# Optimization experiments

Measured on AMD Instinct MI355X. Metric: run time of the kernel, lower is better.

## Reference

```python
import jax, jax.numpy as jnp
import numpy as np

D_MODEL = 1024
N_HEADS = 16
D_HEAD = 64
TOTAL = N_HEADS * D_HEAD


def setup_inputs() -> dict:
    key = jax.random.key(0)
    k1, k2, k3 = jax.random.split(key, 3)
    x = jax.random.normal(k1, (2, 2048, D_MODEL), dtype=jnp.float32)
    W_qkv = jax.random.normal(k2, (3 * TOTAL, D_MODEL), dtype=jnp.float32) * 0.02
    W_out = jax.random.normal(k3, (D_MODEL, TOTAL), dtype=jnp.float32) * 0.02
    return {"x": x, "W_qkv": W_qkv, "W_out": W_out}


def reference(x, W_qkv, W_out):
    B, T, D = x.shape
    scale = D_HEAD ** -0.5
    qkv = jnp.einsum('btd,ed->bte', x, W_qkv)  # [B,T,3*TOTAL]
    q, k, v = jnp.split(qkv, 3, axis=-1)
    def heads(t):
        return t.reshape(B, T, N_HEADS, D_HEAD).transpose(0, 2, 1, 3)  # [B,H,T,Dh]
    q, k, v = heads(q), heads(k), heads(v)
    scores = jnp.einsum('bhqd,bhkd->bhqk', q, k) * scale
    causal = jnp.tril(jnp.ones((T, T), dtype=bool))
    scores = jnp.where(causal[None, None], scores, -jnp.inf)
    attn = jax.nn.softmax(scores, axis=-1)
    out = jnp.einsum('bhqk,bhkd->bhqd', attn, v)
    out = out.transpose(0, 2, 1, 3).reshape(B, T, TOTAL)
    return jnp.einsum('bte,de->btd', out, W_out)
```

## Files before the change

### kernel.cpp

```cpp
#include <hip/hip_runtime.h>
#include <hip/hip_bf16.h>

typedef __attribute__((ext_vector_type(4))) float f32x4;
typedef __attribute__((ext_vector_type(8))) short s16x8;
typedef __attribute__((ext_vector_type(4))) short s16x4;

#define DEV static __device__ __forceinline__

DEV unsigned short f2bf(float f) {
    unsigned int u = __builtin_bit_cast(unsigned int, f);
    u += 0x7fffu + ((u >> 16) & 1u);
    return (unsigned short)(u >> 16);
}

#if __has_builtin(__builtin_amdgcn_exp2f)
#define EXP2(x) __builtin_amdgcn_exp2f(x)
#else
#define EXP2(x) exp2f(x)
#endif

DEV unsigned int pack2(float a, float b) {
#if __has_builtin(__builtin_amdgcn_perm)
    return __builtin_amdgcn_perm(__builtin_bit_cast(unsigned int, b),
                                 __builtin_bit_cast(unsigned int, a), 0x07060302u);
#else
    return (__builtin_bit_cast(unsigned int, a) >> 16) |
           (__builtin_bit_cast(unsigned int, b) & 0xffff0000u);
#endif
}

DEV s16x8 ld8(const unsigned short* p) {
    s16x4 lo = *(const s16x4*)(p);
    s16x4 hi = *(const s16x4*)(p + 4);
    return __builtin_shufflevector(lo, hi, 0, 1, 2, 3, 4, 5, 6, 7);
}
DEV s16x8 ld8a(const unsigned short* p) { return *(const s16x8*)p; }

DEV f32x4 mfma16(s16x8 a, s16x8 b, f32x4 c) {
    return __builtin_amdgcn_mfma_f32_16x16x32_bf16(a, b, c, 0, 0, 0);
}

DEV void glds16(const unsigned short* g, unsigned short* l) {
    __builtin_amdgcn_global_load_lds(
        (const __attribute__((address_space(1))) unsigned int*)g,
        (__attribute__((address_space(3))) unsigned int*)l, 16, 0, 0);
}

__global__ __launch_bounds__(256) void convf2b2(
        const float* __restrict__ s0, unsigned short* __restrict__ d0, int n40,
        const float* __restrict__ s1, unsigned short* __restrict__ d1, int n41) {
    int i = blockIdx.x * 256 + threadIdx.x;
    if (i < n40) {
        float4 v = ((const float4*)s0)[i];
        s16x4 o = {(short)f2bf(v.x), (short)f2bf(v.y), (short)f2bf(v.z), (short)f2bf(v.w)};
        ((s16x4*)d0)[i] = o;
    } else if (i - n40 < n41) {
        int j = i - n40;
        float4 v = ((const float4*)s1)[j];
        s16x4 o = {(short)f2bf(v.x), (short)f2bf(v.y), (short)f2bf(v.z), (short)f2bf(v.w)};
        ((s16x4*)d1)[j] = o;
    }
}

__global__ __launch_bounds__(256) void convf2b(const float* __restrict__ s,
                                               unsigned short* __restrict__ d, int n4) {
    int i = blockIdx.x * 256 + threadIdx.x;
    if (i < n4) {
        float4 v = ((const float4*)s)[i];
        s16x4 o = {(short)f2bf(v.x), (short)f2bf(v.y), (short)f2bf(v.z), (short)f2bf(v.w)};
        ((s16x4*)d)[i] = o;
    }
}

__global__ __launch_bounds__(512) void qkv_gemm(
        const unsigned short* __restrict__ Xb, const unsigned short* __restrict__ Wq,
        unsigned short* __restrict__ q_ws, unsigned short* __restrict__ k_ws,
        unsigned short* __restrict__ v_ws) {
    __shared__ unsigned short As[2][128 * 32];
    __shared__ unsigned short Bs[2][128 * 32];
    const int tid = threadIdx.x, lane = tid & 63, wave = tid >> 6;
    const int l15 = lane & 15, l4 = lane >> 4;
    const int wm = (wave >> 1) * 32, wn = (wave & 1) * 64;
    const int m0 = blockIdx.y * 128, n0 = blockIdx.x * 128;

    f32x4 acc[2][4];
    for (int i = 0; i < 2; i++)
        for (int j = 0; j < 4; j++) acc[i][j] = (f32x4){0.f, 0.f, 0.f, 0.f};

    const unsigned short* aptr = &Xb[(size_t)(m0 + wave * 16 + (lane >> 2)) * 1024 + (lane & 3) * 8];
    const unsigned short* bptr = &Wq[(size_t)(n0 + wave * 16 + (lane >> 2)) * 1024 + (lane & 3) * 8];

    for (int k0 = 0; k0 < 1024; k0 += 64) {
        __syncthreads();
        for (int c = 0; c < 2; c++) {
            glds16(aptr + k0 + c * 32, &As[c][(wave * 16) * 32]);
            glds16(bptr + k0 + c * 32, &Bs[c][(wave * 16) * 32]);
        }
        __syncthreads();
        for (int c = 0; c < 2; c++) {
            s16x8 af[2], bf[4];
            for (int mt = 0; mt < 2; mt++) af[mt] = ld8a(&As[c][(wm + mt * 16 + l15) * 32 + l4 * 8]);
            for (int nt = 0; nt < 4; nt++) bf[nt] = ld8a(&Bs[c][(wn + nt * 16 + l15) * 32 + l4 * 8]);
            for (int mt = 0; mt < 2; mt++)
                for (int nt = 0; nt < 4; nt++)
                    acc[mt][nt] = mfma16(af[mt], bf[nt], acc[mt][nt]);
        }
    }

    const int gnb = n0 + wn;
    const int which = gnb >> 10, h = (gnb >> 6) & 15;
    const int bidx = m0 >> 11, tb = m0 & 2047;
    if (which == 2) {
        unsigned short* dst = v_ws + (size_t)(bidx * 16 + h) * 64 * 2048;
        for (int mt = 0; mt < 2; mt++) {
            int t = tb + wm + mt * 16 + l4 * 4;
            for (int nt = 0; nt < 4; nt++) {
                int dh = nt * 16 + l15;
                s16x4 pp;
                for (int r = 0; r < 4; r++) pp[r] = (short)f2bf(acc[mt][nt][r]);
                *(s16x4*)&dst[(size_t)dh * 2048 + t] = pp;
            }
        }
    } else {
        unsigned short* dst = ((which == 0) ? q_ws : k_ws) + (size_t)(bidx * 16 + h) * 2048 * 64;
        const float sc = (which == 0) ? 0.18033688f : 1.0f;
        for (int mt = 0; mt < 2; mt++) {
            int t0 = tb + wm + mt * 16 + l4 * 4;
            for (int nt = 0; nt < 4; nt++) {
                int dh = nt * 16 + l15;
                for (int r = 0; r < 4; r++)
                    dst[(size_t)(t0 + r) * 64 + dh] = f2bf(acc[mt][nt][r] * sc);
            }
        }
    }
}

__global__ __launch_bounds__(512, 4) void attn(
        const unsigned short* __restrict__ q_ws, const unsigned short* __restrict__ k_ws,
        const unsigned short* __restrict__ v_ws, unsigned short* __restrict__ ao) {
    constexpr int LDP = 68;
    __shared__ unsigned short Ks[3][2][64 * 32];
    __shared__ unsigned short Vt[3][2][64 * 32];
    __shared__ unsigned short Ps[8 * 16 * LDP];
    const int tid = threadIdx.x, lane = tid & 63, wave = tid >> 6;
    const int l15 = lane & 15, l4 = lane >> 4;
    const int xf = (l15 >> 1) & 3;

    const int id = blockIdx.x;
    const int bh8 = id & 7, rest = id >> 3;
    const int qq = rest & 15, g = rest >> 4;
    const int bh = bh8 + 8 * g, b = bh >> 4, h = bh & 15;
    const int p = (g < 2) ? qq : 15 - qq;
    const int qrow = ((wave < 4) ? (31 - p) : p) * 64 + (wave & 3) * 16;
    const int nt = 32 - p;

    const size_t base = (size_t)bh * 2048 * 64;
    const unsigned short* vtb = v_ws + (size_t)bh * 64 * 2048;
    unsigned short* Pw = &Ps[wave * 16 * LDP];

    const int seg = wave >> 1, hf = wave & 1;
    const int srow = lane >> 2;
    const int scol = ((lane & 3) ^ ((lane >> 3) & 3)) * 8;
    const unsigned short* kg = &k_ws[base + (size_t)(seg * 16 + srow) * 64 + hf * 32 + scol];
    const unsigned short* vg = &vtb[(size_t)(seg * 16 + srow) * 2048 + hf * 32 + scol];
    unsigned short* kld = &Ks[0][hf][(seg * 16) * 32];
    unsigned short* vld = &Vt[0][hf][(seg * 16) * 32];
    const unsigned short* krd = &Ks[0][0][0];
    const unsigned short* vrd = &Vt[0][0][0];

    s16x8 qf[2];
    for (int c = 0; c < 2; c++)
        qf[c] = ld8a(&q_ws[base + (size_t)(qrow + l15) * 64 + c * 32 + l4 * 8]);
    asm volatile("s_waitcnt vmcnt(0)" ::: "memory");

    f32x4 o[4];
    for (int i = 0; i < 4; i++) o[i] = (f32x4){0.f, 0.f, 0.f, 0.f};
    float lsum = 0.f;

    glds16(kg, kld);
    glds16(vg, vld);
    glds16(kg + 4096, kld + 4096);
    glds16(vg + 64, vld + 4096);

    int cur = 0;
    for (int r = 0; r < nt; ++r) {
        if (r + 1 < nt) asm volatile("s_waitcnt vmcnt(2)" ::: "memory");
        else            asm volatile("s_waitcnt vmcnt(0)" ::: "memory");
        __builtin_amdgcn_s_barrier();
        if (r + 2 < nt) {
            const int nb = (cur == 0) ? 2 : cur - 1;
            glds16(kg + (size_t)(r + 2) * 4096, kld + nb * 4096);
            glds16(vg + (r + 2) * 64,           vld + nb * 4096);
        }
        const int k0 = r * 64;
        if (k0 < qrow + 16) {
            const unsigned short* kb = krd + cur * 4096;
            const unsigned short* vb = vrd + cur * 4096;
            f32x4 st[4];
            for (int ks = 0; ks < 4; ks++) st[ks] = (f32x4){0.f, 0.f, 0.f, 0.f};
            __builtin_amdgcn_s_setprio(1);
            for (int c = 0; c < 2; c++)
                for (int ks = 0; ks < 4; ks++) {
                    s16x8 kf = ld8a(&kb[c * 2048 + (ks * 16 + l15) * 32 + (l4 ^ xf) * 8]);
                    st[ks] = mfma16(kf, qf[c], st[ks]);
                }
            __builtin_amdgcn_s_setprio(0);

            if (k0 + 63 > qrow) {
                int qg = qrow + l15;
                for (int ks = 0; ks < 4; ks++)
                    for (int rr = 0; rr < 4; rr++) {
                        int kgi = k0 + ks * 16 + l4 * 4 + rr;
                        if (kgi > qg) st[ks][rr] = -1e30f;
                    }
            }
            float part = 0.f;
            for (int ks = 0; ks < 4; ks++) {
                float p0 = EXP2(st[ks][0]);
                float p1 = EXP2(st[ks][1]);
                float p2 = EXP2(st[ks][2]);
                float p3 = EXP2(st[ks][3]);
                part += (p0 + p1) + (p2 + p3);
                unsigned int u0 = pack2(p0, p1), u1 = pack2(p2, p3);
                *(uint2*)&Pw[l15 * LDP + ks * 16 + l4 * 4] = (uint2){u0, u1};
            }
            lsum += part;

            s16x8 pf[2];
            for (int c = 0; c < 2; c++)
                pf[c] = ld8(&Pw[l15 * LDP + c * 32 + l4 * 8]);
            __builtin_amdgcn_s_setprio(1);
            for (int c = 0; c < 2; c++)
                for (int ds = 0; ds < 4; ds++) {
                    s16x8 vf = ld8a(&vb[c * 2048 + (ds * 16 + l15) * 32 + (l4 ^ xf) * 8]);
                    o[ds] = mfma16(vf, pf[c], o[ds]);
                }
            __builtin_amdgcn_s_setprio(0);
        }
        cur = (cur == 2) ? 0 : cur + 1;
    }

    float t = lsum;
    t += __shfl_xor(t, 16, 64);
    t += __shfl_xor(t, 32, 64);
    float inv = 1.f / t;
    for (int ds = 0; ds < 4; ds++) {
        s16x4 pp;
        for (int r = 0; r < 4; r++) pp[r] = (short)f2bf(o[ds][r] * inv);
        *(s16x4*)&Pw[l15 * LDP + ds * 16 + l4 * 4] = pp;
    }
    int qr = lane >> 2, qt = lane & 3;
    size_t orow = ((size_t)b * 2048 + qrow + qr) * 1024 + h * 64 + qt * 16;
    *(s16x8*)&ao[orow]     = ld8(&Pw[qr * LDP + qt * 16]);
    *(s16x8*)&ao[orow + 8] = ld8(&Pw[qr * LDP + qt * 16 + 8]);
}

__global__ __launch_bounds__(256) void out_gemm(
        const unsigned short* __restrict__ A, const unsigned short* __restrict__ Bm,
        float* __restrict__ OUT) {
    __shared__ unsigned short As[2][128 * 32];
    __shared__ unsigned short Bs[2][64 * 32];
    const int tid = threadIdx.x, lane = tid & 63, wave = tid >> 6;
    const int l15 = lane & 15, l4 = lane >> 4;
    const int wm = wave * 32;
    const int m0 = blockIdx.y * 128, n0 = blockIdx.x * 64;

    f32x4 acc[2][4];
    for (int i = 0; i < 2; i++)
        for (int j = 0; j < 4; j++) acc[i][j] = (f32x4){0.f, 0.f, 0.f, 0.f};

    const unsigned short* aptr = &A[(size_t)(m0 + wave * 32 + (lane >> 2)) * 1024 + (lane & 3) * 8];
    const unsigned short* bptr = &Bm[(size_t)(n0 + wave * 16 + (lane >> 2)) * 1024 + (lane & 3) * 8];

    for (int k0 = 0; k0 < 1024; k0 += 64) {
        __syncthreads();
        for (int c = 0; c < 2; c++) {
            glds16(aptr + k0 + c * 32, &As[c][(wave * 32) * 32]);
            glds16(aptr + k0 + c * 32 + 16 * 1024, &As[c][(wave * 32 + 16) * 32]);
            glds16(bptr + k0 + c * 32, &Bs[c][(wave * 16) * 32]);
        }
        __syncthreads();
        for (int c = 0; c < 2; c++) {
            s16x8 af[2], bf[4];
            for (int mt = 0; mt < 2; mt++) af[mt] = ld8a(&As[c][(wm + mt * 16 + l15) * 32 + l4 * 8]);
            for (int nt = 0; nt < 4; nt++) bf[nt] = ld8a(&Bs[c][(nt * 16 + l15) * 32 + l4 * 8]);
            for (int mt = 0; mt < 2; mt++)
                for (int nt = 0; nt < 4; nt++)
                    acc[mt][nt] = mfma16(af[mt], bf[nt], acc[mt][nt]);
        }
    }

    for (int mt = 0; mt < 2; mt++)
        for (int nt = 0; nt < 4; nt++)
            for (int r = 0; r < 4; r++) {
                int gm = m0 + wm + mt * 16 + l4 * 4 + r;
                int gn = n0 + nt * 16 + l15;
                OUT[(size_t)gm * 1024 + gn] = acc[mt][nt][r];
            }
}

extern "C" void kernel_launch(void* const* d_in, const int* in_sizes, int n_in,
                              void* d_out, int out_size, void* d_ws, size_t ws_size,
                              hipStream_t stream) {
    (void)in_sizes; (void)n_in; (void)out_size; (void)ws_size;
    const float* x    = (const float*)d_in[0];
    const float* Wqkv = (const float*)d_in[1];
    const float* Wout = (const float*)d_in[2];
    float* out = (float*)d_out;

    unsigned short* q_ws = (unsigned short*)d_ws;
    unsigned short* k_ws = q_ws + (size_t)4 * 1024 * 1024;
    unsigned short* v_ws = k_ws + (size_t)4 * 1024 * 1024;
    unsigned short* xb   = v_ws + (size_t)4 * 1024 * 1024;
    unsigned short* ao   = xb;
    unsigned short* wqb  = (unsigned short*)d_out;
    unsigned short* wob  = q_ws;

    const int n4x = 2 * 2048 * 1024 / 4, n4w = 3072 * 1024 / 4;
    convf2b2<<<(n4x + n4w + 255) / 256, 256, 0, stream>>>(x, xb, n4x, Wqkv, wqb, n4w);
    qkv_gemm<<<dim3(24, 32), 512, 0, stream>>>(xb, wqb, q_ws, k_ws, v_ws);
    attn<<<dim3(512), 512, 0, stream>>>(q_ws, k_ws, v_ws, ao);
    convf2b<<<1024, 256, 0, stream>>>(Wout, wob, 1024 * 1024 / 4);
    out_gemm<<<dim3(16, 32), 256, 0, stream>>>(ao, wob, out);
}
```

Before: 165.0 us.

## Enlarge QKV GEMM tiles to 256x256 with swizzled LDS and pipelined loads

Rewrites the QKV projection GEMM to use 256x256 output tiles with a K-step of 64 and double-buffered LDS. Global-to-LDS loads for the next step are issued while MFMAs run on the current one, using explicit vmcnt waits, barriers and setprio. An XOR swizzle on the LDS layout avoids bank conflicts, and the 1D grid of 192 blocks is remapped to group tiles for L2 reuse. The goal is higher arithmetic intensity and better overlap of memory and compute. The cost is 128 KB of LDS per block, more accumulator registers, and only 192 blocks, which may leave some CUs idle.

```diff
diff --git a/kernel.cpp b/kernel.cpp
--- a/kernel.cpp
+++ b/kernel.cpp
@@ -72,64 +72,152 @@
     }
 }
 
-__global__ __launch_bounds__(512) void qkv_gemm(
+__global__ __launch_bounds__(512, 2) void qkv_gemm(
         const unsigned short* __restrict__ Xb, const unsigned short* __restrict__ Wq,
         unsigned short* __restrict__ q_ws, unsigned short* __restrict__ k_ws,
         unsigned short* __restrict__ v_ws) {
-    __shared__ unsigned short As[2][128 * 32];
-    __shared__ unsigned short Bs[2][128 * 32];
+    __shared__ unsigned short As[2][256 * 64];
+    __shared__ unsigned short Bs[2][256 * 64];
     const int tid = threadIdx.x, lane = tid & 63, wave = tid >> 6;
     const int l15 = lane & 15, l4 = lane >> 4;
-    const int wm = (wave >> 1) * 32, wn = (wave & 1) * 64;
-    const int m0 = blockIdx.y * 128, n0 = blockIdx.x * 128;
-
-    f32x4 acc[2][4];
-    for (int i = 0; i < 2; i++)
+    const int wr = wave >> 2, wc = wave & 3;
+    const int swz = (blockIdx.x & 7) * 24 + (blockIdx.x >> 3);
+    const int m0 = (swz / 12) * 256, n0 = (swz % 12) * 256;
+
+    f32x4 acc[8][4];
+#pragma unroll
+    for (int i = 0; i < 8; i++)
+#pragma unroll
         for (int j = 0; j < 4; j++) acc[i][j] = (f32x4){0.f, 0.f, 0.f, 0.f};
 
-    const unsigned short* aptr = &Xb[(size_t)(m0 + wave * 16 + (lane >> 2)) * 1024 + (lane & 3) * 8];
-    const unsigned short* bptr = &Wq[(size_t)(n0 + wave * 16 + (lane >> 2)) * 1024 + (lane & 3) * 8];
-
-    for (int k0 = 0; k0 < 1024; k0 += 64) {
-        __syncthreads();
-        for (int c = 0; c < 2; c++) {
-            glds16(aptr + k0 + c * 32, &As[c][(wave * 16) * 32]);
-            glds16(bptr + k0 + c * 32, &Bs[c][(wave * 16) * 32]);
-        }
-        __syncthreads();
-        for (int c = 0; c < 2; c++) {
-            s16x8 af[2], bf[4];
-            for (int mt = 0; mt < 2; mt++) af[mt] = ld8a(&As[c][(wm + mt * 16 + l15) * 32 + l4 * 8]);
-            for (int nt = 0; nt < 4; nt++) bf[nt] = ld8a(&Bs[c][(wn + nt * 16 + l15) * 32 + l4 * 8]);
-            for (int mt = 0; mt < 2; mt++)
-                for (int nt = 0; nt < 4; nt++)
-                    acc[mt][nt] = mfma16(af[mt], bf[nt], acc[mt][nt]);
-        }
-    }
-
-    const int gnb = n0 + wn;
+    const int srow = lane >> 3, sslot = (lane & 7) ^ srow;
+    const unsigned short* aG = &Xb[(size_t)(m0 + wave * 32 + srow) * 1024 + sslot * 8];
+    const unsigned short* bG = &Wq[(size_t)(n0 + wave * 32 + srow) * 1024 + sslot * 8];
+
+#pragma unroll
+    for (int g = 0; g < 4; g++) glds16(aG + g * 8 * 1024, &As[0][(wave * 32 + g * 8) * 64]);
+#pragma unroll
+    for (int g = 0; g < 4; g++) glds16(bG + g * 8 * 1024, &Bs[0][(wave * 32 + g * 8) * 64]);
+
+    const int xro = l15 & 7;
+    s16x8 bf[4];
+    for (int t = 0; t < 16; ++t) {
+        const unsigned short* Ab = &As[t & 1][0];
+        const unsigned short* Bb = &Bs[t & 1][0];
+        unsigned short* Al = &As[(t & 1) ^ 1][0];
+        unsigned short* Bl = &Bs[(t & 1) ^ 1][0];
+
+        if (t < 15) {
+            const unsigned short* ag = aG + (size_t)(t + 1) * 64;
+#pragma unroll
+            for (int g = 0; g < 4; g++)
+                glds16(ag + g * 8 * 1024, &Al[(wave * 32 + g * 8) * 64]);
+            asm volatile("s_waitcnt vmcnt(4)" ::: "memory");
+        } else {
+            asm volatile("s_waitcnt vmcnt(0)" ::: "memory");
+        }
+        __builtin_amdgcn_s_barrier();
+        {
+            s16x8 af[4];
+#pragma unroll
+            for (int ii = 0; ii < 4; ii++)
+                af[ii] = ld8a(&Ab[(wr * 128 + ii * 16 + l15) * 64 + ((l4 ^ xro) * 8)]);
+#pragma unroll
+            for (int j = 0; j < 4; j++)
+                bf[j] = ld8a(&Bb[(wc * 64 + j * 16 + l15) * 64 + ((l4 ^ xro) * 8)]);
+            __builtin_amdgcn_s_setprio(1);
+#pragma unroll
+            for (int ii = 0; ii < 4; ii++)
+#pragma unroll
+                for (int j = 0; j < 4; j++) acc[ii][j] = mfma16(af[ii], bf[j], acc[ii][j]);
+            __builtin_amdgcn_s_setprio(0);
+        }
+        __builtin_amdgcn_s_barrier();
+
+        {
+            if (t < 15) {
+                const unsigned short* bg = bG + (size_t)(t + 1) * 64;
+#pragma unroll
+                for (int g = 0; g < 4; g++)
+                    glds16(bg + g * 8 * 1024, &Bl[(wave * 32 + g * 8) * 64]);
+            }
+            s16x8 af[4];
+#pragma unroll
+            for (int ii = 0; ii < 4; ii++)
+                af[ii] = ld8a(&Ab[(wr * 128 + (4 + ii) * 16 + l15) * 64 + ((l4 ^ xro) * 8)]);
+            __builtin_amdgcn_s_barrier();
+            __builtin_amdgcn_s_setprio(1);
+#pragma unroll
+            for (int ii = 0; ii < 4; ii++)
+#pragma unroll
+                for (int j = 0; j < 4; j++) acc[4 + ii][j] = mfma16(af[ii], bf[j], acc[4 + ii][j]);
+            __builtin_amdgcn_s_setprio(0);
+        }
+        __builtin_amdgcn_s_barrier();
+
+        {
+            s16x8 af[4];
+#pragma unroll
+            for (int ii = 0; ii < 4; ii++)
+                af[ii] = ld8a(&Ab[(wr * 128 + ii * 16 + l15) * 64 + (((4 + l4) ^ xro) * 8)]);
+#pragma unroll
+            for (int j = 0; j < 4; j++)
+                bf[j] = ld8a(&Bb[(wc * 64 + j * 16 + l15) * 64 + (((4 + l4) ^ xro) * 8)]);
+            __builtin_amdgcn_s_barrier();
+            __builtin_amdgcn_s_setprio(1);
+#pragma unroll
+            for (int ii = 0; ii < 4; ii++)
+#pragma unroll
+                for (int j = 0; j < 4; j++) acc[ii][j] = mfma16(af[ii], bf[j], acc[ii][j]);
+            __builtin_amdgcn_s_setprio(0);
+        }
+        __builtin_amdgcn_s_barrier();
+
+        {
+            s16x8 af[4];
+#pragma unroll
+            for (int ii = 0; ii < 4; ii++)
+                af[ii] = ld8a(&Ab[(wr * 128 + (4 + ii) * 16 + l15) * 64 + (((4 + l4) ^ xro) * 8)]);
+            __builtin_amdgcn_s_barrier();
+            __builtin_amdgcn_s_setprio(1);
+#pragma unroll
+            for (int ii = 0; ii < 4; ii++)
+#pragma unroll
+                for (int j = 0; j < 4; j++) acc[4 + ii][j] = mfma16(af[ii], bf[j], acc[4 + ii][j]);
+            __builtin_amdgcn_s_setprio(0);
+        }
+        __builtin_amdgcn_s_barrier();
+    }
+
+    const int gnb = n0 + wc * 64;
     const int which = gnb >> 10, h = (gnb >> 6) & 15;
     const int bidx = m0 >> 11, tb = m0 & 2047;
     if (which == 2) {
         unsigned short* dst = v_ws + (size_t)(bidx * 16 + h) * 64 * 2048;
-        for (int mt = 0; mt < 2; mt++) {
-            int t = tb + wm + mt * 16 + l4 * 4;
-            for (int nt = 0; nt < 4; nt++) {
-                int dh = nt * 16 + l15;
+#pragma unroll
+        for (int i = 0; i < 8; i++) {
+            int tq = tb + wr * 128 + i * 16 + l4 * 4;
+#pragma unroll
+            for (int j = 0; j < 4; j++) {
+                int dh = j * 16 + l15;
                 s16x4 pp;
-                for (int r = 0; r < 4; r++) pp[r] = (short)f2bf(acc[mt][nt][r]);
-                *(s16x4*)&dst[(size_t)dh * 2048 + t] = pp;
+#pragma unroll
+                for (int r = 0; r < 4; r++) pp[r] = (short)f2bf(acc[i][j][r]);
+                *(s16x4*)&dst[(size_t)dh * 2048 + tq] = pp;
             }
         }
     } else {
         unsigned short* dst = ((which == 0) ? q_ws : k_ws) + (size_t)(bidx * 16 + h) * 2048 * 64;
         const float sc = (which == 0) ? 0.18033688f : 1.0f;
-        for (int mt = 0; mt < 2; mt++) {
-            int t0 = tb + wm + mt * 16 + l4 * 4;
-            for (int nt = 0; nt < 4; nt++) {
-                int dh = nt * 16 + l15;
+#pragma unroll
+        for (int i = 0; i < 8; i++) {
+            int t0 = tb + wr * 128 + i * 16 + l4 * 4;
+#pragma unroll
+            for (int j = 0; j < 4; j++) {
+                int dh = j * 16 + l15;
+#pragma unroll
                 for (int r = 0; r < 4; r++)
-                    dst[(size_t)(t0 + r) * 64 + dh] = f2bf(acc[mt][nt][r] * sc);
+                    dst[(size_t)(t0 + r) * 64 + dh] = f2bf(acc[i][j][r] * sc);
             }
         }
     }
@@ -318,7 +406,7 @@
 
     const int n4x = 2 * 2048 * 1024 / 4, n4w = 3072 * 1024 / 4;
     convf2b2<<<(n4x + n4w + 255) / 256, 256, 0, stream>>>(x, xb, n4x, Wqkv, wqb, n4w);
-    qkv_gemm<<<dim3(24, 32), 512, 0, stream>>>(xb, wqb, q_ws, k_ws, v_ws);
+    qkv_gemm<<<dim3(192), 512, 0, stream>>>(xb, wqb, q_ws, k_ws, v_ws);
     attn<<<dim3(512), 512, 0, stream>>>(q_ws, k_ws, v_ws, ao);
     convf2b<<<1024, 256, 0, stream>>>(Wout, wob, 1024 * 1024 / 4);
     out_gemm<<<dim3(16, 32), 256, 0, stream>>>(ao, wob, out);
```

Result: slower. 184.3 us (+11.7%).

## Process 32 query rows per wave in attention and fold Wout conversion into prologue

Applied to the files above, without the earlier changes.

The attention kernel now gives each wave two 16-row query subtiles, so 128 query rows per block, and halves the grid to 256 blocks. Each K and V fragment read from LDS now feeds two MFMAs, which reuses shared-memory loads and halves global K/V staging per query row. The price is roughly double the accumulator and score registers, lower occupancy (launch bounds drop to 2 blocks) and a bigger P buffer. Separately, when the workspace is large enough, the W_out fp32-to-bf16 conversion is merged into the first conversion kernel to remove one launch.

```diff
diff --git a/kernel.cpp b/kernel.cpp
--- a/kernel.cpp
+++ b/kernel.cpp
@@ -46,9 +46,10 @@
         (__attribute__((address_space(3))) unsigned int*)l, 16, 0, 0);
 }
 
-__global__ __launch_bounds__(256) void convf2b2(
+__global__ __launch_bounds__(256) void convf2b3(
         const float* __restrict__ s0, unsigned short* __restrict__ d0, int n40,
-        const float* __restrict__ s1, unsigned short* __restrict__ d1, int n41) {
+        const float* __restrict__ s1, unsigned short* __restrict__ d1, int n41,
+        const float* __restrict__ s2, unsigned short* __restrict__ d2, int n42) {
     int i = blockIdx.x * 256 + threadIdx.x;
     if (i < n40) {
         float4 v = ((const float4*)s0)[i];
@@ -59,6 +60,11 @@
         float4 v = ((const float4*)s1)[j];
         s16x4 o = {(short)f2bf(v.x), (short)f2bf(v.y), (short)f2bf(v.z), (short)f2bf(v.w)};
         ((s16x4*)d1)[j] = o;
+    } else if (i - n40 - n41 < n42) {
+        int j = i - n40 - n41;
+        float4 v = ((const float4*)s2)[j];
+        s16x4 o = {(short)f2bf(v.x), (short)f2bf(v.y), (short)f2bf(v.z), (short)f2bf(v.w)};
+        ((s16x4*)d2)[j] = o;
     }
 }
 
@@ -135,28 +141,28 @@
     }
 }
 
-__global__ __launch_bounds__(512, 4) void attn(
+__global__ __launch_bounds__(512, 2) void attn(
         const unsigned short* __restrict__ q_ws, const unsigned short* __restrict__ k_ws,
         const unsigned short* __restrict__ v_ws, unsigned short* __restrict__ ao) {
     constexpr int LDP = 68;
     __shared__ unsigned short Ks[3][2][64 * 32];
     __shared__ unsigned short Vt[3][2][64 * 32];
-    __shared__ unsigned short Ps[8 * 16 * LDP];
+    __shared__ unsigned short Ps[8 * 32 * LDP];
     const int tid = threadIdx.x, lane = tid & 63, wave = tid >> 6;
     const int l15 = lane & 15, l4 = lane >> 4;
     const int xf = (l15 >> 1) & 3;
 
     const int id = blockIdx.x;
     const int bh8 = id & 7, rest = id >> 3;
-    const int qq = rest & 15, g = rest >> 4;
+    const int p = rest & 7, g = rest >> 3;
     const int bh = bh8 + 8 * g, b = bh >> 4, h = bh & 15;
-    const int p = (g < 2) ? qq : 15 - qq;
-    const int qrow = ((wave < 4) ? (31 - p) : p) * 64 + (wave & 3) * 16;
-    const int nt = 32 - p;
+    const int chunk = (wave < 4) ? (15 - p) : p;
+    const int qrow = chunk * 128 + (wave & 3) * 32;
+    const int nt = 2 * (16 - p);
 
     const size_t base = (size_t)bh * 2048 * 64;
     const unsigned short* vtb = v_ws + (size_t)bh * 64 * 2048;
-    unsigned short* Pw = &Ps[wave * 16 * LDP];
+    unsigned short* Pw = &Ps[wave * 32 * LDP];
 
     const int seg = wave >> 1, hf = wave & 1;
     const int srow = lane >> 2;
@@ -168,14 +174,20 @@
     const unsigned short* krd = &Ks[0][0][0];
     const unsigned short* vrd = &Vt[0][0][0];
 
-    s16x8 qf[2];
-    for (int c = 0; c < 2; c++)
-        qf[c] = ld8a(&q_ws[base + (size_t)(qrow + l15) * 64 + c * 32 + l4 * 8]);
+    s16x8 qf[2][2];
+#pragma unroll
+    for (int qs = 0; qs < 2; qs++)
+#pragma unroll
+        for (int c = 0; c < 2; c++)
+            qf[qs][c] = ld8a(&q_ws[base + (size_t)(qrow + qs * 16 + l15) * 64 + c * 32 + l4 * 8]);
     asm volatile("s_waitcnt vmcnt(0)" ::: "memory");
 
-    f32x4 o[4];
-    for (int i = 0; i < 4; i++) o[i] = (f32x4){0.f, 0.f, 0.f, 0.f};
-    float lsum = 0.f;
+    f32x4 o[2][4];
+#pragma unroll
+    for (int qs = 0; qs < 2; qs++)
+#pragma unroll
+        for (int i = 0; i < 4; i++) o[qs][i] = (f32x4){0.f, 0.f, 0.f, 0.f};
+    float lsum[2] = {0.f, 0.f};
 
     glds16(kg, kld);
     glds16(vg, vld);
@@ -196,63 +208,90 @@
         if (k0 < qrow + 16) {
             const unsigned short* kb = krd + cur * 4096;
             const unsigned short* vb = vrd + cur * 4096;
-            f32x4 st[4];
-            for (int ks = 0; ks < 4; ks++) st[ks] = (f32x4){0.f, 0.f, 0.f, 0.f};
+            f32x4 st[2][4];
+#pragma unroll
+            for (int qs = 0; qs < 2; qs++)
+#pragma unroll
+                for (int ks = 0; ks < 4; ks++) st[qs][ks] = (f32x4){0.f, 0.f, 0.f, 0.f};
             __builtin_amdgcn_s_setprio(1);
+#pragma unroll
             for (int c = 0; c < 2; c++)
+#pragma unroll
                 for (int ks = 0; ks < 4; ks++) {
                     s16x8 kf = ld8a(&kb[c * 2048 + (ks * 16 + l15) * 32 + (l4 ^ xf) * 8]);
-                    st[ks] = mfma16(kf, qf[c], st[ks]);
+                    st[0][ks] = mfma16(kf, qf[0][c], st[0][ks]);
+                    st[1][ks] = mfma16(kf, qf[1][c], st[1][ks]);
                 }
             __builtin_amdgcn_s_setprio(0);
 
-            if (k0 + 63 > qrow) {
-                int qg = qrow + l15;
-                for (int ks = 0; ks < 4; ks++)
-                    for (int rr = 0; rr < 4; rr++) {
-                        int kgi = k0 + ks * 16 + l4 * 4 + rr;
-                        if (kgi > qg) st[ks][rr] = -1e30f;
-                    }
+#pragma unroll
+            for (int qs = 0; qs < 2; qs++) {
+                const int qb = qrow + qs * 16;
+                if (k0 + 63 > qb) {
+                    int qg = qb + l15;
+#pragma unroll
+                    for (int ks = 0; ks < 4; ks++)
+#pragma unroll
+                        for (int rr = 0; rr < 4; rr++) {
+                            int kgi = k0 + ks * 16 + l4 * 4 + rr;
+                            if (kgi > qg) st[qs][ks][rr] = -1e30f;
+                        }
+                }
+                float part = 0.f;
+#pragma unroll
+                for (int ks = 0; ks < 4; ks++) {
+                    float p0 = EXP2(st[qs][ks][0]);
+                    float p1 = EXP2(st[qs][ks][1]);
+                    float p2 = EXP2(st[qs][ks][2]);
+                    float p3 = EXP2(st[qs][ks][3]);
+                    part += (p0 + p1) + (p2 + p3);
+                    unsigned int u0 = pack2(p0, p1), u1 = pack2(p2, p3);
+                    *(uint2*)&Pw[(qs * 16 + l15) * LDP + ks * 16 + l4 * 4] = (uint2){u0, u1};
+                }
+                lsum[qs] += part;
             }
-            float part = 0.f;
-            for (int ks = 0; ks < 4; ks++) {
-                float p0 = EXP2(st[ks][0]);
-                float p1 = EXP2(st[ks][1]);
-                float p2 = EXP2(st[ks][2]);
-                float p3 = EXP2(st[ks][3]);
-                part += (p0 + p1) + (p2 + p3);
-                unsigned int u0 = pack2(p0, p1), u1 = pack2(p2, p3);
-                *(uint2*)&Pw[l15 * LDP + ks * 16 + l4 * 4] = (uint2){u0, u1};
-            }
-            lsum += part;
-
-            s16x8 pf[2];
+
+            s16x8 pf[2][2];
+#pragma unroll
+            for (int qs = 0; qs < 2; qs++)
+#pragma unroll
+                for (int c = 0; c < 2; c++)
+                    pf[qs][c] = ld8(&Pw[(qs * 16 + l15) * LDP + c * 32 + l4 * 8]);
+            __builtin_amdgcn_s_setprio(1);
+#pragma unroll
             for (int c = 0; c < 2; c++)
-                pf[c] = ld8(&Pw[l15 * LDP + c * 32 + l4 * 8]);
-            __builtin_amdgcn_s_setprio(1);
-            for (int c = 0; c < 2; c++)
+#pragma unroll
                 for (int ds = 0; ds < 4; ds++) {
                     s16x8 vf = ld8a(&vb[c * 2048 + (ds * 16 + l15) * 32 + (l4 ^ xf) * 8]);
-                    o[ds] = mfma16(vf, pf[c], o[ds]);
+                    o[0][ds] = mfma16(vf, pf[0][c], o[0][ds]);
+                    o[1][ds] = mfma16(vf, pf[1][c], o[1][ds]);
                 }
             __builtin_amdgcn_s_setprio(0);
         }
         cur = (cur == 2) ? 0 : cur + 1;
     }
 
-    float t = lsum;
-    t += __shfl_xor(t, 16, 64);
-    t += __shfl_xor(t, 32, 64);
-    float inv = 1.f / t;
-    for (int ds = 0; ds < 4; ds++) {
-        s16x4 pp;
-        for (int r = 0; r < 4; r++) pp[r] = (short)f2bf(o[ds][r] * inv);
-        *(s16x4*)&Pw[l15 * LDP + ds * 16 + l4 * 4] = pp;
+#pragma unroll
+    for (int qs = 0; qs < 2; qs++) {
+        float t = lsum[qs];
+        t += __shfl_xor(t, 16, 64);
+        t += __shfl_xor(t, 32, 64);
+        float inv = 1.f / t;
+#pragma unroll
+        for (int ds = 0; ds < 4; ds++) {
+            s16x4 pp;
+#pragma unroll
+            for (int r = 0; r < 4; r++) pp[r] = (short)f2bf(o[qs][ds][r] * inv);
+            *(s16x4*)&Pw[(qs * 16 + l15) * LDP + ds * 16 + l4 * 4] = pp;
+        }
     }
     int qr = lane >> 2, qt = lane & 3;
-    size_t orow = ((size_t)b * 2048 + qrow + qr) * 1024 + h * 64 + qt * 16;
-    *(s16x8*)&ao[orow]     = ld8(&Pw[qr * LDP + qt * 16]);
-    *(s16x8*)&ao[orow + 8] = ld8(&Pw[qr * LDP + qt * 16 + 8]);
+#pragma unroll
+    for (int qs = 0; qs < 2; qs++) {
+        size_t orow = ((size_t)b * 2048 + qrow + qs * 16 + qr) * 1024 + h * 64 + qt * 16;
+        *(s16x8*)&ao[orow]     = ld8(&Pw[(qs * 16 + qr) * LDP + qt * 16]);
+        *(s16x8*)&ao[orow + 8] = ld8(&Pw[(qs * 16 + qr) * LDP + qt * 16 + 8]);
+    }
 }
 
 __global__ __launch_bounds__(256) void out_gemm(
@@ -302,7 +341,7 @@
 extern "C" void kernel_launch(void* const* d_in, const int* in_sizes, int n_in,
                               void* d_out, int out_size, void* d_ws, size_t ws_size,
                               hipStream_t stream) {
-    (void)in_sizes; (void)n_in; (void)out_size; (void)ws_size;
+    (void)in_sizes; (void)n_in; (void)out_size;
     const float* x    = (const float*)d_in[0];
     const float* Wqkv = (const float*)d_in[1];
     const float* Wout = (const float*)d_in[2];
@@ -314,12 +353,21 @@
     unsigned short* xb   = v_ws + (size_t)4 * 1024 * 1024;
     unsigned short* ao   = xb;
     unsigned short* wqb  = (unsigned short*)d_out;
-    unsigned short* wob  = q_ws;
-
-    const int n4x = 2 * 2048 * 1024 / 4, n4w = 3072 * 1024 / 4;
-    convf2b2<<<(n4x + n4w + 255) / 256, 256, 0, stream>>>(x, xb, n4x, Wqkv, wqb, n4w);
+
+    const int n4x = 2 * 2048 * 1024 / 4, n4w = 3072 * 1024 / 4, n4o = 1024 * 1024 / 4;
+    const bool merged = ws_size >= (size_t)35 * 1024 * 1024;
+    unsigned short* wob = merged ? (q_ws + (size_t)16 * 1024 * 1024)
+                                 : q_ws;
+
+    if (merged) {
+        convf2b3<<<(n4x + n4w + n4o + 255) / 256, 256, 0, stream>>>(
+            x, xb, n4x, Wqkv, wqb, n4w, Wout, wob, n4o);
+    } else {
+        convf2b3<<<(n4x + n4w + 255) / 256, 256, 0, stream>>>(
+            x, xb, n4x, Wqkv, wqb, n4w, Wout, wob, 0);
+    }
     qkv_gemm<<<dim3(24, 32), 512, 0, stream>>>(xb, wqb, q_ws, k_ws, v_ws);
-    attn<<<dim3(512), 512, 0, stream>>>(q_ws, k_ws, v_ws, ao);
-    convf2b<<<1024, 256, 0, stream>>>(Wout, wob, 1024 * 1024 / 4);
+    attn<<<dim3(256), 512, 0, stream>>>(q_ws, k_ws, v_ws, ao);
+    if (!merged) convf2b<<<1024, 256, 0, stream>>>(Wout, wob, n4o);
     out_gemm<<<dim3(16, 32), 256, 0, stream>>>(ao, wob, out);
 }
```

Measured after the change: 175.4 us. +6.3%, slower.
